# Kernel tuning notes

Measured on AMD Instinct MI355X. Metric: run time of the kernel, lower is better.

## Reference

```python
import jax, jax.numpy as jnp
import numpy as np

B, E, S, H = 8, 1024, 2048, 16  # batch, embed_dim, seq_len, n_heads
D = E // H                       # per-head hidden dim


def setup_inputs() -> dict:
    key = jax.random.key(0)
    k1, k2 = jax.random.split(key)
    x = jax.random.normal(k1, (B, E, S), dtype=jnp.float32)
    weight = jax.random.normal(k2, (H, S), dtype=jnp.float32)  # nn.Parameter(torch.randn)
    bias = jnp.zeros((H, S), dtype=jnp.float32)                # nn.Parameter(torch.zeros)
    return {"x": x, "weight": weight, "bias": bias}


def _vector_to_matrix(v):
    # v: (H, S) -> M: (H, S, S), M[h, i, j] = v[h, j - i] if j >= i else 0
    h, m = v.shape
    i = jnp.arange(m)[:, None]
    j = jnp.arange(m)[None, :]
    off = j - i  # negative offsets wrap (same as torch fancy indexing) but are masked out
    return jnp.where(j >= i, v[:, off], jnp.zeros((), dtype=v.dtype))


def reference(x, weight, bias):
    b, e, s = x.shape
    h = weight.shape[0]
    d = e // h
    M = _vector_to_matrix(weight)  # (H, S, S)
    # Original: x.view(B,H,D,S).reshape(B*H,D,S) paired with W.repeat_interleave(B,0),
    # i.e. flat index k uses M[k // B]. Group the flat B*H axis into H contiguous
    # blocks of size B so each block shares one Toeplitz matrix (no (B*H,S,S) blowup).
    xg = x.reshape(b * h, d, s).reshape(h, b, d, s)  # block m = M[m]
    out = jnp.einsum('mbds,mst->mbdt', xg, M) + bias[:, None, None, :]
    return out.reshape(b, e, s)
```

## Files before the change

### kernel.cpp

```cpp
#include <hip/hip_runtime.h>
#include <hip/hip_bf16.h>

#define SEQ    2048
#define NHEAD  16
#define RPH    512
#define BM     128
#define BK     64
#define NTH    512

#define WSTRIDE 2184
#define ABUF_E  8192
#define WCOP_E  (2 * ABUF_E)
#define TOT_E   (WCOP_E + 8 * WSTRIDE + 128)

typedef float  f32x4  __attribute__((ext_vector_type(4)));
typedef __bf16 bf16x8 __attribute__((ext_vector_type(8)));

struct PF { float4 v0, v1, v2, v3; };

__device__ __forceinline__ unsigned f2bf(float f) {
    union { __hip_bfloat16 h; unsigned short u; } cv;
    cv.h = __float2bfloat16(f);
    return (unsigned)cv.u;
}

__device__ __forceinline__ uint4 pack8u(float4 a, float4 b) {
    union { bf16x8 v; uint4 u; } r;
    r.v[0] = (__bf16)a.x; r.v[1] = (__bf16)a.y;
    r.v[2] = (__bf16)a.z; r.v[3] = (__bf16)a.w;
    r.v[4] = (__bf16)b.x; r.v[5] = (__bf16)b.y;
    r.v[6] = (__bf16)b.z; r.v[7] = (__bf16)b.w;
    return r.u;
}

#define MFMA16(a, b, c) __builtin_amdgcn_mfma_f32_16x16x32_bf16((a), (b), (c), 0, 0, 0)

#define LOADPF(P, CH)                                                         \
  { const float* g_ = Xp + (size_t)(CH) * BK;                                 \
    P.v0 = *(const float4*)g_;                                                \
    P.v1 = *(const float4*)(g_ + 4);                                          \
    P.v2 = *(const float4*)(g_ + 8);                                          \
    P.v3 = *(const float4*)(g_ + 12); }

#define WRITEA(AB, P)                                                         \
  { *(uint4*)((AB) + wb0) = pack8u(P.v0, P.v1);                               \
    *(uint4*)((AB) + wb1) = pack8u(P.v2, P.v3); }

#define KSTEP0(ABC)                                                           \
  { const int kb_ = kq16 ^ swz;                                               \
    bf16x8 af0 = *(const bf16x8*)((ABC) + Arow0 + kb_);                       \
    bf16x8 af1 = *(const bf16x8*)((ABC) + Arow1 + kb_);                       \
    acc[0][0] = MFMA16(af0, bw[7], acc[0][0]);                                \
    acc[1][0] = MFMA16(af1, bw[7], acc[1][0]);                                \
    acc[0][1] = MFMA16(af0, bw[6], acc[0][1]);                                \
    acc[1][1] = MFMA16(af1, bw[6], acc[1][1]);                                \
    acc[0][2] = MFMA16(af0, bw[5], acc[0][2]);                                \
    acc[1][2] = MFMA16(af1, bw[5], acc[1][2]);                                \
    acc[0][3] = MFMA16(af0, bw[4], acc[0][3]);                                \
    acc[1][3] = MFMA16(af1, bw[4], acc[1][3]);                                \
    acc[0][4] = MFMA16(af0, bw[3], acc[0][4]);                                \
    acc[1][4] = MFMA16(af1, bw[3], acc[1][4]);                                \
    acc[0][5] = MFMA16(af0, bw[2], acc[0][5]);                                \
    acc[1][5] = MFMA16(af1, bw[2], acc[1][5]);                                \
    acc[0][6] = MFMA16(af0, bw[1], acc[0][6]);                                \
    acc[1][6] = MFMA16(af1, bw[1], acc[1][6]);                                \
    acc[0][7] = MFMA16(af0, bw[0], acc[0][7]);                                \
    acc[1][7] = MFMA16(af1, bw[0], acc[1][7]); }

#define KSTEP1(ABC)                                                           \
  { const int kb_ = (64 + kq16) ^ swz;                                        \
    bf16x8 af0 = *(const bf16x8*)((ABC) + Arow0 + kb_);                       \
    bf16x8 af1 = *(const bf16x8*)((ABC) + Arow1 + kb_);                       \
    acc[0][7] = MFMA16(af0, bw[2], acc[0][7]);                                \
    acc[1][7] = MFMA16(af1, bw[2], acc[1][7]);                                \
    acc[0][6] = MFMA16(af0, bw[3], acc[0][6]);                                \
    acc[1][6] = MFMA16(af1, bw[3], acc[1][6]);                                \
    acc[0][5] = MFMA16(af0, bw[4], acc[0][5]);                                \
    acc[1][5] = MFMA16(af1, bw[4], acc[1][5]);                                \
    acc[0][4] = MFMA16(af0, bw[5], acc[0][4]);                                \
    acc[1][4] = MFMA16(af1, bw[5], acc[1][4]);                                \
    acc[0][3] = MFMA16(af0, bw[6], acc[0][3]);                                \
    acc[1][3] = MFMA16(af1, bw[6], acc[1][3]);                                \
    acc[0][2] = MFMA16(af0, bw[7], acc[0][2]);                                \
    acc[1][2] = MFMA16(af1, bw[7], acc[1][2]);                                \
    acc[0][1] = MFMA16(af0, bw[0], acc[0][1]);                                \
    acc[1][1] = MFMA16(af1, bw[0], acc[1][1]);                                \
    acc[0][0] = MFMA16(af0, bw[1], acc[0][0]);                                \
    acc[1][0] = MFMA16(af1, bw[1], acc[1][0]); }

#define CHUNKBODY(CH, ABC, ABN)                                               \
  {                                                                           \
    WRITEA(ABN, pf);                         \
    if ((CH) + 2 < nch) LOADPF(pf, (CH) + 2);                                 \
    if ((CH) < nchw) {                                                        \
      const unsigned short* bq_ = wcB + 64 * (CH) - 112;                      \
      bw[0] = *(const bf16x8*)(bq_);                                          \
      bw[1] = *(const bf16x8*)(bq_ + 16);                                     \
      bw[2] = *(const bf16x8*)(bq_ + 32);                                     \
      bw[3] = *(const bf16x8*)(bq_ + 48);                                     \
      bw[4] = *(const bf16x8*)(bq_ + 64);                                     \
      bw[5] = *(const bf16x8*)(bq_ + 80);                                     \
      bw[6] = *(const bf16x8*)(bq_ + 96);                                     \
      bw[7] = *(const bf16x8*)(bq_ + 112);                                    \
      __builtin_amdgcn_s_setprio(1);                                          \
      KSTEP0(ABC);                                                            \
      bw[0] = *(const bf16x8*)(bq_ + 128);                        \
      bw[1] = *(const bf16x8*)(bq_ + 144);                        \
      KSTEP1(ABC);                                                            \
      __builtin_amdgcn_s_setprio(0);                                          \
    }                                                                         \
    asm volatile("s_waitcnt lgkmcnt(0)\n\ts_barrier" ::: "memory");           \
  }

__global__ __launch_bounds__(NTH, 4) void mixer_kernel(
    const float* __restrict__ x, const float* __restrict__ wgt,
    const float* __restrict__ bias, float* __restrict__ out)
{
    __shared__ unsigned short smem[TOT_E] __attribute__((aligned(16)));
    char* ab0 = (char*)smem;
    char* ab1 = (char*)smem + ABUF_E * 2;
    unsigned short* wc = smem + WCOP_E;

    const int tid  = threadIdx.x;
    const int lane = tid & 63;
    const int wv   = tid >> 6;
    const int r    = wv & 3;
    const int tb   = wv >> 2;

    const int bid  = blockIdx.x;
    const int m    = (bid & 7) + 8 * ((bid >> 3) & 1);
    const int rt   = (bid >> 4) & 3;
    const int j    = 7 - (bid >> 6);
    const int nch  = 4 * j + 4;
    const int nchw = nch - 2 + 2 * tb;

    const float* Xb = x   + (size_t)(m * RPH + rt * BM) * SEQ;
    float*       Ob = out + (size_t)(m * RPH + rt * BM) * SEQ;
    const float* wr = wgt  + m * SEQ;
    const float* br = bias + m * SEQ;

    const int srow = 32 * r + 16 * tb + (lane >> 2);
    const int colq = lane & 3;
    const int wsw  = (srow & 7) << 4;
    const int wb0  = srow * 128 + ((colq * 32) ^ wsw);
    const int wb1  = srow * 128 + ((colq * 32 + 16) ^ wsw);
    const float* Xp = Xb + (size_t)srow * SEQ + colq * 16;

    PF pf;
    LOADPF(pf, 0);

    if (tid < 256) {
        const int t8 = tid * 8;
        const float* g = wr + (2040 - t8);
        float4 lo = *(const float4*)g;
        float4 hi = *(const float4*)(g + 4);
        uint4 v;
        v.x = f2bf(hi.w) | (f2bf(hi.z) << 16);
        v.y = f2bf(hi.y) | (f2bf(hi.x) << 16);
        v.z = f2bf(lo.w) | (f2bf(lo.z) << 16);
        v.w = f2bf(lo.y) | (f2bf(lo.x) << 16);
        *(uint4*)(smem + 8 + t8) = v;
        if (tid < 21) {
            uint4 z = {0u, 0u, 0u, 0u};
            unsigned short* dst = (tid == 0) ? smem
                                 : smem + 8 + 2048 + (tid - 1) * 8;
            *(uint4*)dst = z;
        }
    }
    __syncthreads();

    #pragma unroll
    for (int c = 0; c < 8; ++c) {
        for (int grp = tid; grp < WSTRIDE / 8; grp += NTH) {
            const int i = grp * 8;
            uint4 g0 = *(const uint4*)(smem + 8 + i - 8);
            uint4 g1 = *(const uint4*)(smem + 8 + i);
            unsigned d[9] = {g0.x, g0.y, g0.z, g0.w,
                             g1.x, g1.y, g1.z, g1.w, 0u};
            const int qd = (16 - 2 * c) >> 2;
            uint4 o;
            if (c & 1) {
                o.x = (d[qd]     >> 16) | (d[qd + 1] << 16);
                o.y = (d[qd + 1] >> 16) | (d[qd + 2] << 16);
                o.z = (d[qd + 2] >> 16) | (d[qd + 3] << 16);
                o.w = (d[qd + 3] >> 16) | (d[qd + 4] << 16);
            } else {
                o.x = d[qd];     o.y = d[qd + 1];
                o.z = d[qd + 2]; o.w = d[qd + 3];
            }
            *(uint4*)(wc + c * WSTRIDE + i) = o;
        }
    }
    __syncthreads();

    const int col_low = lane & 15;
    const int kq      = lane >> 4;
    const int kq16    = kq * 16;
    const int swz     = (col_low & 7) << 4;
    const int rbw     = 32 * r;
    const int t0w     = 256 * j + 128 * tb;
    const int cpy     = (col_low + 1) & 7;
    const int BcBase  = cpy * WSTRIDE + cpy + 2047 - col_low + 8 * kq;
    const int Arow0   = (rbw      + col_low) * 128;
    const int Arow1   = (rbw + 16 + col_low) * 128;
    const unsigned short* wcB = wc + (BcBase - t0w);

    WRITEA(ab0, pf);
    LOADPF(pf, 1);
    __syncthreads();

    bf16x8 bw[8];
    f32x4 acc[2][8] = {};
    for (int ch = 0; ch < nch; ch += 2) {
        CHUNKBODY(ch,     ab0, ab1);
        CHUNKBODY(ch + 1, ab1, ab0);
    }

    #pragma unroll
    for (int c = 0; c < 8; ++c) {
        const int colg = t0w + 16 * c + col_low;
        const float bv = br[colg];
        #pragma unroll
        for (int a = 0; a < 2; ++a) {
            const int rowl = rbw + 16 * a + 4 * kq;
            #pragma unroll
            for (int rr = 0; rr < 4; ++rr)
                Ob[(size_t)(rowl + rr) * SEQ + colg] = acc[a][c][rr] + bv;
        }
    }
}

extern "C" void kernel_launch(void* const* d_in, const int* in_sizes, int n_in,
                              void* d_out, int out_size, void* d_ws, size_t ws_size,
                              hipStream_t stream) {
    const float* x  = (const float*)d_in[0];
    const float* w  = (const float*)d_in[1];
    const float* bs = (const float*)d_in[2];
    float* out = (float*)d_out;
    dim3 grid(512);
    dim3 block(NTH);
    hipLaunchKernelGGL(mixer_kernel, grid, block, 0, stream, x, w, bs, out);
}
```

Before: 43.95 us.

## Shrink row tile to 32 with paired column blocks and rotating Toeplitz register window

Reworks the block decomposition: each 256-thread block now handles 32 rows and two 512-column output blocks, paired (3 with 0, 2 with 1) so every block does roughly the same amount of causal work. The Toeplitz weight fragments live in a 16-entry rotating register window, so each chunk loads only the new fragments instead of reloading all eight. The goal is to balance load across blocks and cut redundant LDS reads of the weights. In exchange, the per-block A tile is smaller, giving less A reuse, and occupancy hints drop to 2 blocks per CU with smaller blocks.

```diff
diff --git a/kernel.cpp b/kernel.cpp
--- a/kernel.cpp
+++ b/kernel.cpp
@@ -4,19 +4,18 @@
 #define SEQ    2048
 #define NHEAD  16
 #define RPH    512
-#define BM     128
 #define BK     64
-#define NTH    512
+#define NTH    256
 
 #define WSTRIDE 2184
-#define ABUF_E  8192
+#define ABUF_E  2048
 #define WCOP_E  (2 * ABUF_E)
-#define TOT_E   (WCOP_E + 8 * WSTRIDE + 128)
+#define TOT_E   (WCOP_E + 8 * WSTRIDE)
 
 typedef float  f32x4  __attribute__((ext_vector_type(4)));
 typedef __bf16 bf16x8 __attribute__((ext_vector_type(8)));
 
-struct PF { float4 v0, v1, v2, v3; };
+struct PF { float4 v0, v1; };
 
 __device__ __forceinline__ unsigned f2bf(float f) {
     union { __hip_bfloat16 h; unsigned short u; } cv;
@@ -38,81 +37,51 @@
 #define LOADPF(P, CH)                                                         \
   { const float* g_ = Xp + (size_t)(CH) * BK;                                 \
     P.v0 = *(const float4*)g_;                                                \
-    P.v1 = *(const float4*)(g_ + 4);                                          \
-    P.v2 = *(const float4*)(g_ + 8);                                          \
-    P.v3 = *(const float4*)(g_ + 12); }
-
-#define WRITEA(AB, P)                                                         \
-  { *(uint4*)((AB) + wb0) = pack8u(P.v0, P.v1);                               \
-    *(uint4*)((AB) + wb1) = pack8u(P.v2, P.v3); }
-
-#define KSTEP0(ABC)                                                           \
-  { const int kb_ = kq16 ^ swz;                                               \
+    P.v1 = *(const float4*)(g_ + 4); }
+
+#define WRITEA(AB, P)  { *(uint4*)((AB) + wb0) = pack8u(P.v0, P.v1); }
+
+#define KSTEPQ(ABC, KS, P)                                                    \
+  { const int kb_ = (64 * (KS) + kq16) ^ swz;                                 \
     bf16x8 af0 = *(const bf16x8*)((ABC) + Arow0 + kb_);                       \
     bf16x8 af1 = *(const bf16x8*)((ABC) + Arow1 + kb_);                       \
-    acc[0][0] = MFMA16(af0, bw[7], acc[0][0]);                                \
-    acc[1][0] = MFMA16(af1, bw[7], acc[1][0]);                                \
-    acc[0][1] = MFMA16(af0, bw[6], acc[0][1]);                                \
-    acc[1][1] = MFMA16(af1, bw[6], acc[1][1]);                                \
-    acc[0][2] = MFMA16(af0, bw[5], acc[0][2]);                                \
-    acc[1][2] = MFMA16(af1, bw[5], acc[1][2]);                                \
-    acc[0][3] = MFMA16(af0, bw[4], acc[0][3]);                                \
-    acc[1][3] = MFMA16(af1, bw[4], acc[1][3]);                                \
-    acc[0][4] = MFMA16(af0, bw[3], acc[0][4]);                                \
-    acc[1][4] = MFMA16(af1, bw[3], acc[1][4]);                                \
-    acc[0][5] = MFMA16(af0, bw[2], acc[0][5]);                                \
-    acc[1][5] = MFMA16(af1, bw[2], acc[1][5]);                                \
-    acc[0][6] = MFMA16(af0, bw[1], acc[0][6]);                                \
-    acc[1][6] = MFMA16(af1, bw[1], acc[1][6]);                                \
-    acc[0][7] = MFMA16(af0, bw[0], acc[0][7]);                                \
-    acc[1][7] = MFMA16(af1, bw[0], acc[1][7]); }
-
-#define KSTEP1(ABC)                                                           \
-  { const int kb_ = (64 + kq16) ^ swz;                                        \
-    bf16x8 af0 = *(const bf16x8*)((ABC) + Arow0 + kb_);                       \
-    bf16x8 af1 = *(const bf16x8*)((ABC) + Arow1 + kb_);                       \
-    acc[0][7] = MFMA16(af0, bw[2], acc[0][7]);                                \
-    acc[1][7] = MFMA16(af1, bw[2], acc[1][7]);                                \
-    acc[0][6] = MFMA16(af0, bw[3], acc[0][6]);                                \
-    acc[1][6] = MFMA16(af1, bw[3], acc[1][6]);                                \
-    acc[0][5] = MFMA16(af0, bw[4], acc[0][5]);                                \
-    acc[1][5] = MFMA16(af1, bw[4], acc[1][5]);                                \
-    acc[0][4] = MFMA16(af0, bw[5], acc[0][4]);                                \
-    acc[1][4] = MFMA16(af1, bw[5], acc[1][4]);                                \
-    acc[0][3] = MFMA16(af0, bw[6], acc[0][3]);                                \
-    acc[1][3] = MFMA16(af1, bw[6], acc[1][3]);                                \
-    acc[0][2] = MFMA16(af0, bw[7], acc[0][2]);                                \
-    acc[1][2] = MFMA16(af1, bw[7], acc[1][2]);                                \
-    acc[0][1] = MFMA16(af0, bw[0], acc[0][1]);                                \
-    acc[1][1] = MFMA16(af1, bw[0], acc[1][1]);                                \
-    acc[0][0] = MFMA16(af0, bw[1], acc[0][0]);                                \
-    acc[1][0] = MFMA16(af1, bw[1], acc[1][0]); }
-
-#define CHUNKBODY(CH, ABC, ABN)                                               \
+    acc[0][0] = MFMA16(af0, bw[((P)+2*(KS)-0)&15], acc[0][0]);                \
+    acc[1][0] = MFMA16(af1, bw[((P)+2*(KS)-0)&15], acc[1][0]);                \
+    acc[0][1] = MFMA16(af0, bw[((P)+2*(KS)-1)&15], acc[0][1]);                \
+    acc[1][1] = MFMA16(af1, bw[((P)+2*(KS)-1)&15], acc[1][1]);                \
+    acc[0][2] = MFMA16(af0, bw[((P)+2*(KS)-2)&15], acc[0][2]);                \
+    acc[1][2] = MFMA16(af1, bw[((P)+2*(KS)-2)&15], acc[1][2]);                \
+    acc[0][3] = MFMA16(af0, bw[((P)+2*(KS)-3)&15], acc[0][3]);                \
+    acc[1][3] = MFMA16(af1, bw[((P)+2*(KS)-3)&15], acc[1][3]);                \
+    acc[0][4] = MFMA16(af0, bw[((P)+2*(KS)-4)&15], acc[0][4]);                \
+    acc[1][4] = MFMA16(af1, bw[((P)+2*(KS)-4)&15], acc[1][4]);                \
+    acc[0][5] = MFMA16(af0, bw[((P)+2*(KS)-5)&15], acc[0][5]);                \
+    acc[1][5] = MFMA16(af1, bw[((P)+2*(KS)-5)&15], acc[1][5]);                \
+    acc[0][6] = MFMA16(af0, bw[((P)+2*(KS)-6)&15], acc[0][6]);                \
+    acc[1][6] = MFMA16(af1, bw[((P)+2*(KS)-6)&15], acc[1][6]);                \
+    acc[0][7] = MFMA16(af0, bw[((P)+2*(KS)-7)&15], acc[0][7]);                \
+    acc[1][7] = MFMA16(af1, bw[((P)+2*(KS)-7)&15], acc[1][7]); }
+
+#define CHUNKBODY(CH, P, ABC, ABN)                                            \
   {                                                                           \
     WRITEA(ABN, pf);                         \
     if ((CH) + 2 < nch) LOADPF(pf, (CH) + 2);                                 \
     if ((CH) < nchw) {                                                        \
-      const unsigned short* bq_ = wcB + 64 * (CH) - 112;                      \
-      bw[0] = *(const bf16x8*)(bq_);                                          \
-      bw[1] = *(const bf16x8*)(bq_ + 16);                                     \
-      bw[2] = *(const bf16x8*)(bq_ + 32);                                     \
-      bw[3] = *(const bf16x8*)(bq_ + 48);                                     \
-      bw[4] = *(const bf16x8*)(bq_ + 64);                                     \
-      bw[5] = *(const bf16x8*)(bq_ + 80);                                     \
-      bw[6] = *(const bf16x8*)(bq_ + 96);                                     \
-      bw[7] = *(const bf16x8*)(bq_ + 112);                                    \
       __builtin_amdgcn_s_setprio(1);                                          \
-      KSTEP0(ABC);                                                            \
-      bw[0] = *(const bf16x8*)(bq_ + 128);                        \
-      bw[1] = *(const bf16x8*)(bq_ + 144);                        \
-      KSTEP1(ABC);                                                            \
+      KSTEPQ(ABC, 0, P);                                                      \
+      bw[((P)+1)&15] = *(const bf16x8*)(wcB + 64 * (CH) + 16);                \
+      bw[((P)+2)&15] = *(const bf16x8*)(wcB + 64 * (CH) + 32);                \
+      KSTEPQ(ABC, 1, P);                                                      \
       __builtin_amdgcn_s_setprio(0);                                          \
+    }                                                                         \
+    if ((CH) + 1 < nchw) {                                                    \
+      bw[((P)+3)&15] = *(const bf16x8*)(wcB + 64 * (CH) + 48);                \
+      bw[((P)+4)&15] = *(const bf16x8*)(wcB + 64 * (CH) + 64);                \
     }                                                                         \
     asm volatile("s_waitcnt lgkmcnt(0)\n\ts_barrier" ::: "memory");           \
   }
 
-__global__ __launch_bounds__(NTH, 4) void mixer_kernel(
+__global__ __launch_bounds__(NTH, 2) void mixer_kernel(
     const float* __restrict__ x, const float* __restrict__ wgt,
     const float* __restrict__ bias, float* __restrict__ out)
 {
@@ -123,33 +92,29 @@
 
     const int tid  = threadIdx.x;
     const int lane = tid & 63;
-    const int wv   = tid >> 6;
-    const int r    = wv & 3;
-    const int tb   = wv >> 2;
+    const int tb   = tid >> 6;
 
     const int bid  = blockIdx.x;
     const int m    = (bid & 7) + 8 * ((bid >> 3) & 1);
-    const int rt   = (bid >> 4) & 3;
-    const int j    = 7 - (bid >> 6);
-    const int nch  = 4 * j + 4;
-    const int nchw = nch - 2 + 2 * tb;
-
-    const float* Xb = x   + (size_t)(m * RPH + rt * BM) * SEQ;
-    float*       Ob = out + (size_t)(m * RPH + rt * BM) * SEQ;
+    const int rt   = (bid >> 4) & 15;
+    const int pc   = bid >> 8;
+    const int qA   = pc ? 2 : 3;
+    const int qB   = pc ? 1 : 0;
+
+    const float* Xb = x   + (size_t)(m * RPH + rt * 32) * SEQ;
+    float*       Ob = out + (size_t)(m * RPH + rt * 32) * SEQ;
     const float* wr = wgt  + m * SEQ;
     const float* br = bias + m * SEQ;
 
-    const int srow = 32 * r + 16 * tb + (lane >> 2);
-    const int colq = lane & 3;
+    const int srow = tid >> 3;
     const int wsw  = (srow & 7) << 4;
-    const int wb0  = srow * 128 + ((colq * 32) ^ wsw);
-    const int wb1  = srow * 128 + ((colq * 32 + 16) ^ wsw);
-    const float* Xp = Xb + (size_t)srow * SEQ + colq * 16;
+    const int wb0  = srow * 128 + (((tid & 7) * 16) ^ wsw);
+    const float* Xp = Xb + (size_t)srow * SEQ + (tid & 7) * 8;
 
     PF pf;
     LOADPF(pf, 0);
 
-    if (tid < 256) {
+    {
         const int t8 = tid * 8;
         const float* g = wr + (2040 - t8);
         float4 lo = *(const float4*)g;
@@ -197,35 +162,48 @@
     const int kq      = lane >> 4;
     const int kq16    = kq * 16;
     const int swz     = (col_low & 7) << 4;
-    const int rbw     = 32 * r;
-    const int t0w     = 256 * j + 128 * tb;
     const int cpy     = (col_low + 1) & 7;
     const int BcBase  = cpy * WSTRIDE + cpy + 2047 - col_low + 8 * kq;
-    const int Arow0   = (rbw      + col_low) * 128;
-    const int Arow1   = (rbw + 16 + col_low) * 128;
-    const unsigned short* wcB = wc + (BcBase - t0w);
-
-    WRITEA(ab0, pf);
-    LOADPF(pf, 1);
-    __syncthreads();
-
-    bf16x8 bw[8];
-    f32x4 acc[2][8] = {};
-    for (int ch = 0; ch < nch; ch += 2) {
-        CHUNKBODY(ch,     ab0, ab1);
-        CHUNKBODY(ch + 1, ab1, ab0);
-    }
-
-    #pragma unroll
-    for (int c = 0; c < 8; ++c) {
-        const int colg = t0w + 16 * c + col_low;
-        const float bv = br[colg];
+    const int Arow0   = col_low * 128;
+    const int Arow1   = (col_low + 16) * 128;
+
+    for (int h = 0; h < 2; ++h) {
+        const int q    = h ? qB : qA;
+        const int nch  = 8 * q + 8;
+        const int nchw = 8 * q + 2 * tb + 2;
+        const int t0w  = 512 * q + 128 * tb;
+        const unsigned short* wcB = wc + (BcBase - t0w);
+
+        if (h) LOADPF(pf, 0);
+
+        bf16x8 bw[16];
         #pragma unroll
-        for (int a = 0; a < 2; ++a) {
-            const int rowl = rbw + 16 * a + 4 * kq;
+        for (int w = -7; w <= 0; ++w)
+            bw[w & 15] = *(const bf16x8*)(wcB + 16 * w);
+
+        WRITEA(ab0, pf);
+        LOADPF(pf, 1);
+        asm volatile("s_waitcnt lgkmcnt(0)\n\ts_barrier" ::: "memory");
+
+        f32x4 acc[2][8] = {};
+        for (int ch = 0; ch < nch; ch += 4) {
+            CHUNKBODY(ch,      0, ab0, ab1);
+            CHUNKBODY(ch + 1,  4, ab1, ab0);
+            CHUNKBODY(ch + 2,  8, ab0, ab1);
+            CHUNKBODY(ch + 3, 12, ab1, ab0);
+        }
+
+        #pragma unroll
+        for (int c = 0; c < 8; ++c) {
+            const int colg = t0w + 16 * c + col_low;
+            const float bv = br[colg];
             #pragma unroll
-            for (int rr = 0; rr < 4; ++rr)
-                Ob[(size_t)(rowl + rr) * SEQ + colg] = acc[a][c][rr] + bv;
+            for (int a = 0; a < 2; ++a) {
+                const int rowl = 16 * a + 4 * kq;
+                #pragma unroll
+                for (int rr = 0; rr < 4; ++rr)
+                    Ob[(size_t)(rowl + rr) * SEQ + colg] = acc[a][c][rr] + bv;
+            }
         }
     }
 }
```

Result: no change. 44.00 us (+0.1%).
